# Kernel optimization log

Measured on AMD Instinct MI355X. Metric: run time of the kernel, lower is better.

The kernel has to match this reference:

```python
import jax, jax.numpy as jnp
import numpy as np

DIM = 4096
NH = 32       # query heads
NKV = 8       # kv heads
HD = DIM // NH  # 128
B = 1
S = 2048
ROPE_BASE = 10000.0


def rope_tables(seq_len, head_dim, base=ROPE_BASE):
    inv_freq = 1.0 / base ** (jnp.arange(0, head_dim, 2, dtype=jnp.float32) / head_dim)
    t = jnp.arange(seq_len, dtype=jnp.float32)
    freqs = jnp.einsum('i,j->ij', t, inv_freq)          # [S, HD/2]
    emb = jnp.concatenate([freqs, freqs], axis=-1)      # [S, HD]
    return jnp.cos(emb), jnp.sin(emb)


def apply_rope(x, cos, sin):
    # x: [B, H, S, HD]; matches torch apply_rotary_emb (chunk halves)
    x1, x2 = jnp.split(x, 2, axis=-1)
    d = x1.shape[-1]
    c = cos[None, None, :, :d]
    s = sin[None, None, :, :d]
    return jnp.concatenate([x1 * c - x2 * s, x2 * c + x1 * s], axis=-1)


def setup_inputs() -> dict:
    key = jax.random.key(0)
    k0, k1, k2, k3, k4 = jax.random.split(key, 5)
    sc = 0.02  # typical init scale for stable softmax
    return {
        'x': jax.random.normal(k0, (B, S, DIM), jnp.float32),
        'wq': jax.random.normal(k1, (DIM, NH * HD), jnp.float32) * sc,
        'wk': jax.random.normal(k2, (DIM, NKV * HD), jnp.float32) * sc,
        'wv': jax.random.normal(k3, (DIM, NKV * HD), jnp.float32) * sc,
        'wo': jax.random.normal(k4, (NH * HD, DIM), jnp.float32) * sc,
        'mask': jnp.ones((1,), jnp.bool_),  # presence triggers is_causal=True in torch SDPA path
    }


def reference(x, wq, wk, wv, wo, mask):
    Bsz, Sl, _ = x.shape
    n_rep = NH // NKV
    q = (x @ wq).reshape(Bsz, Sl, NH, HD).transpose(0, 2, 1, 3)    # [B,NH,S,HD]
    k = (x @ wk).reshape(Bsz, Sl, NKV, HD).transpose(0, 2, 1, 3)   # [B,NKV,S,HD]
    v = (x @ wv).reshape(Bsz, Sl, NKV, HD).transpose(0, 2, 1, 3)
    cos, sin = rope_tables(Sl, HD)
    q = apply_rope(q, cos, sin)
    k = apply_rope(k, cos, sin)
    # GQA without repeat_interleave: group query heads per kv head
    qg = q.reshape(Bsz, NKV, n_rep, Sl, HD)
    scale = HD ** -0.5
    scores = jnp.einsum('bgrqd,bgkd->bgrqk', qg, k) * scale        # [B,NKV,n_rep,S,S]
    causal = jnp.tril(jnp.ones((Sl, Sl), dtype=bool))
    scores = jnp.where(causal[None, None, None], scores, jnp.finfo(scores.dtype).min)
    attn = jax.nn.softmax(scores, axis=-1)
    out = jnp.einsum('bgrqk,bgkd->bgrqd', attn, v)                 # [B,NKV,n_rep,S,HD]
    out = out.reshape(Bsz, NH, Sl, HD).transpose(0, 2, 1, 3).reshape(Bsz, Sl, NH * HD)
    return out @ wo
```

## Files before the change

### kernel.cpp

```cpp
#include <hip/hip_runtime.h>
#include <hip/hip_bf16.h>
#include <cstdint>
#include <cmath>

#define DIM 4096
#define NH 32
#define NKV 8
#define HD 128
#define S_LEN 2048
#define KVD (NKV * HD)
#define QS 6144
#define SCALE 0.08838834764831845f

typedef __attribute__((ext_vector_type(4))) float f32x4;
typedef __attribute__((ext_vector_type(8))) short short8;

__device__ __forceinline__ short f2bf(float f) {
  union { float f; uint32_t u; } v; v.f = f;
  uint32_t u = v.u;
  u += 0x7fffu + ((u >> 16) & 1u);
  return (short)(u >> 16);
}
__device__ __forceinline__ float bf2f(short b) {
  union { uint32_t u; float f; } v; v.u = ((uint32_t)(uint16_t)b) << 16;
  return v.f;
}

__device__ __forceinline__ void async16(const void* g, void* l) {
  __builtin_amdgcn_global_load_lds(
      (__attribute__((address_space(1))) void*)(g),
      (__attribute__((address_space(3))) void*)(l), 16, 0, 0);
}


__global__ void rope_tables_k(float* __restrict__ ct, float* __restrict__ st) {
  const int i = blockIdx.x * blockDim.x + threadIdx.x;
  if (i >= S_LEN * 64) return;
  const int s = i >> 6, d = i & 63;
  const float inv = powf(10000.0f, -(float)(2 * d) / 128.0f);
  const float fr = (float)s * inv;
  ct[i] = cosf(fr);
  st[i] = sinf(fr);
}

__global__ void cast_f32_bf16_k(const float* __restrict__ in, short* __restrict__ out, int n4) {
  const int i = blockIdx.x * blockDim.x + threadIdx.x;
  if (i >= n4) return;
  const float4 v = ((const float4*)in)[i];
  short4 o;
  o.x = f2bf(v.x); o.y = f2bf(v.y); o.z = f2bf(v.z); o.w = f2bf(v.w);
  ((short4*)out)[i] = o;
}

__global__ __launch_bounds__(256) void prep_w_k(
    const float* __restrict__ wq, const float* __restrict__ wk,
    const float* __restrict__ wv, const float* __restrict__ wo,
    short* __restrict__ wqkvT, short* __restrict__ woT) {
  __shared__ float tile[64][65];
  int b = blockIdx.x;
  const float* src; short* dst; int N, bx, by;
  if (b < 4096)      { src = wq; dst = wqkvT;                        N = 4096; bx = b & 63; by = b >> 6; }
  else if (b < 5120) { b -= 4096; src = wk; dst = wqkvT + (size_t)4096 * DIM; N = 1024; bx = b & 15; by = b >> 4; }
  else if (b < 6144) { b -= 5120; src = wv; dst = wqkvT + (size_t)5120 * DIM; N = 1024; bx = b & 15; by = b >> 4; }
  else               { b -= 6144; src = wo; dst = woT;               N = 4096; bx = b & 63; by = b >> 6; }
  const int r0 = by * 64, c0 = bx * 64;
  const int t = threadIdx.x;
  const int lr = t >> 4, lc = (t & 15) * 4;
#pragma unroll
  for (int j = 0; j < 4; ++j) {
    const float4 v = *(const float4*)(src + (size_t)(r0 + lr + j * 16) * N + c0 + lc);
    tile[lr + j * 16][lc + 0] = v.x;
    tile[lr + j * 16][lc + 1] = v.y;
    tile[lr + j * 16][lc + 2] = v.z;
    tile[lr + j * 16][lc + 3] = v.w;
  }
  __syncthreads();
  const int orr = (t & 7) * 8;
  const int oc0 = t >> 3;
#pragma unroll
  for (int j = 0; j < 2; ++j) {
    const int oc = oc0 + j * 32;
    short8 o;
#pragma unroll
    for (int k = 0; k < 8; ++k) o[k] = f2bf(tile[orr + k][oc]);
    *(short8*)(dst + (size_t)(c0 + oc) * DIM + r0 + orr) = o;
  }
}

__global__ void transpose_bf16_k(const short* __restrict__ in, short* __restrict__ out,
                                 int R, int C, int ldi) {
  __shared__ short tile[32][33];
  const int tx = threadIdx.x, ty = threadIdx.y;
  const int c0 = blockIdx.x * 32, r0 = blockIdx.y * 32;
#pragma unroll
  for (int j = 0; j < 4; ++j)
    tile[ty + j * 8][tx] = in[(size_t)(r0 + ty + j * 8) * ldi + c0 + tx];
  __syncthreads();
#pragma unroll
  for (int j = 0; j < 4; ++j)
    out[(size_t)(c0 + ty + j * 8) * R + r0 + tx] = tile[tx][ty + j * 8];
}

__global__ void rope_apply_k(short* __restrict__ xq, int ld, const float* __restrict__ ct,
                             const float* __restrict__ st, int nheads) {
  const int i = blockIdx.x * blockDim.x + threadIdx.x;
  const int total = S_LEN * nheads * 64;
  if (i >= total) return;
  const int d = i & 63;
  const int t = i >> 6;
  const int hh = t % nheads;
  const int s = t / nheads;
  short* p = xq + (size_t)s * ld + hh * HD + d;
  const float x1 = bf2f(p[0]);
  const float x2 = bf2f(p[64]);
  const float c = ct[(s << 6) + d];
  const float sn = st[(s << 6) + d];
  p[0]  = f2bf(x1 * c - x2 * sn);
  p[64] = f2bf(x2 * c + x1 * sn);
}

#define SYNC2(VM, LG)                                            \
  asm volatile("s_waitcnt vmcnt(" #VM ")" ::: "memory");         \
  __builtin_amdgcn_s_barrier();                                  \
  asm volatile("s_waitcnt lgkmcnt(" #LG ")" ::: "memory");       \
  __builtin_amdgcn_sched_barrier(0);                             \
  __builtin_amdgcn_s_setprio(1)

#define PH_END()                                                 \
  __builtin_amdgcn_s_setprio(0);                                 \
  __builtin_amdgcn_sched_barrier(0);                             \
  __builtin_amdgcn_s_barrier()


__global__ __launch_bounds__(512, 2) void gemm192_k(
    const short* __restrict__ A, const short* __restrict__ BT,
    short* __restrict__ C, int M, int N, int K) {
  __shared__ __attribute__((aligned(16))) short ldsA[2][256 * 64];
  __shared__ __attribute__((aligned(16))) short ldsB[2][192 * 64];
  const int tid = threadIdx.x;
  const int l = tid & 63, w = tid >> 6;
  const int wrM = w >> 1, wcN = w & 1;
  const int lrow = l & 15, lg = l >> 4;
  const int cofs[2] = {(lg ^ (lrow & 7)) << 3, ((4 + lg) ^ (lrow & 7)) << 3};
  (void)M;

  int bid = blockIdx.x;
  const int cpx = gridDim.x >> 3;
  bid = (bid & 7) * cpx + (bid >> 3);
  const int ntn = N / 192;
  const int m0 = (bid / ntn) << 8;
  const int n0 = (bid % ntn) * 192;

  auto stageA = [&](int tau) {
    const int k0 = tau << 6;
    short* ad = &ldsA[tau & 1][0];
#pragma unroll
    for (int it = 0; it < 4; ++it) {
      const int e = it * 512 + tid;
      const int row = e >> 3;
      const int js = (e & 7) ^ (row & 7);
      async16(A + (size_t)(m0 + row) * K + k0 + js * 8, ad + e * 8);
    }
  };
  auto stageB = [&](int tau) {
    const int k0 = tau << 6;
    short* bd = &ldsB[tau & 1][0];
#pragma unroll
    for (int it = 0; it < 3; ++it) {
      const int e = it * 512 + tid;
      const int row = e >> 3;
      const int js = (e & 7) ^ (row & 7);
      async16(BT + (size_t)(n0 + row) * K + k0 + js * 8, bd + e * 8);
    }
  };
  auto rdA = [&](short8 (&dst)[4][2], int b) {
    const short* p = &ldsA[b][0];
#pragma unroll
    for (int mi = 0; mi < 4; ++mi) {
      const int row = wrM * 64 + mi * 16 + lrow;
#pragma unroll
      for (int kk = 0; kk < 2; ++kk)
        dst[mi][kk] = *(const short8*)(p + row * 64 + cofs[kk]);
    }
  };
  auto rdB3 = [&](short8 (&dst)[3][2], int b, int h) {
    const short* p = &ldsB[b][0];
#pragma unroll
    for (int ni = 0; ni < 3; ++ni) {
      const int row = wcN * 96 + h * 48 + ni * 16 + lrow;
#pragma unroll
      for (int kk = 0; kk < 2; ++kk)
        dst[ni][kk] = *(const short8*)(p + row * 64 + cofs[kk]);
    }
  };

  f32x4 acc[4][6] = {};
  auto half24 = [&](short8 (&Af)[4][2], int h, short8 (&Bf)[3][2]) {
#pragma unroll
    for (int kk = 0; kk < 2; ++kk)
#pragma unroll
      for (int mi = 0; mi < 4; ++mi)
#pragma unroll
        for (int ni = 0; ni < 3; ++ni)
          acc[mi][h * 3 + ni] = __builtin_amdgcn_mfma_f32_16x16x32_bf16(
              Af[mi][kk], Bf[ni][kk], acc[mi][h * 3 + ni], 0, 0, 0);
  };

  short8 Aa[4][2], Ab[4][2], BF[3][2], BS[3][2];

  stageA(0); stageB(0); stageA(1); stageB(1);
  asm volatile("s_waitcnt vmcnt(7)" ::: "memory");
  __builtin_amdgcn_s_barrier();
  rdA(Aa, 0); rdB3(BF, 0, 0);

  const int KT = K >> 6;
  for (int u = 0; u < (KT - 2) / 2; ++u) {
    const int e = 2 * u;
    rdB3(BS, 0, 1);
    SYNC2(7, 6);  stageA(e + 2); half24(Aa, 0, BF); PH_END();
    SYNC2(4, 0);  stageB(e + 2); rdA(Ab, 1); rdB3(BF, 1, 0);
                  half24(Aa, 1, BS); PH_END();
    rdB3(BS, 1, 1);
    SYNC2(7, 6);  stageA(e + 3); half24(Ab, 0, BF); PH_END();
    SYNC2(4, 0);  stageB(e + 3); rdA(Aa, 0); rdB3(BF, 0, 0);
                  half24(Ab, 1, BS); PH_END();
  }
  rdB3(BS, 0, 1);
  SYNC2(7, 6);  half24(Aa, 0, BF); PH_END();
  SYNC2(0, 0);  rdA(Ab, 1); rdB3(BF, 1, 0);
                half24(Aa, 1, BS); PH_END();
  rdB3(BS, 1, 1);
  SYNC2(0, 6);  half24(Ab, 0, BF); PH_END();
  SYNC2(0, 0);  half24(Ab, 1, BS); PH_END();

  const int orow0 = m0 + wrM * 64 + lg * 4;
  const int ocol0 = n0 + wcN * 96 + lrow;
#pragma unroll
  for (int mi = 0; mi < 4; ++mi)
#pragma unroll
    for (int n = 0; n < 6; ++n)
#pragma unroll
      for (int r = 0; r < 4; ++r)
        C[(size_t)(orow0 + mi * 16 + r) * N + (ocol0 + n * 16)] = f2bf(acc[mi][n][r]);
}


__global__ __launch_bounds__(512, 2) void gemm_wo2_k(
    const short* __restrict__ A, const short* __restrict__ BT,
    float* __restrict__ C, int M, int N, int K) {
  __shared__ __attribute__((aligned(16))) short ldsA[2][128 * 64];
  __shared__ __attribute__((aligned(16))) short ldsB[2][256 * 64];
  const int tid = threadIdx.x;
  const int l = tid & 63, w = tid >> 6;
  const int wrM = w >> 2, wcN = w & 3;
  const int lrow = l & 15, lg = l >> 4;
  const int cofs[2] = {(lg ^ (lrow & 7)) << 3, ((4 + lg) ^ (lrow & 7)) << 3};
  (void)M;

  int bid = blockIdx.x;
  const int cpx = gridDim.x >> 3;
  bid = (bid & 7) * cpx + (bid >> 3);
  const int ntn = N >> 8;
  const int m0 = (bid / ntn) << 7;
  const int n0 = (bid % ntn) << 8;

  auto stageA2 = [&](int tau) {
    const int k0 = tau << 6;
    short* ad = &ldsA[tau & 1][0];
#pragma unroll
    for (int it = 0; it < 2; ++it) {
      const int e = it * 512 + tid;
      const int row = e >> 3;
      const int js = (e & 7) ^ (row & 7);
      async16(A + (size_t)(m0 + row) * K + k0 + js * 8, ad + e * 8);
    }
  };
  auto stageB2 = [&](int tau) {
    const int k0 = tau << 6;
    short* bd = &ldsB[tau & 1][0];
#pragma unroll
    for (int it = 0; it < 4; ++it) {
      const int e = it * 512 + tid;
      const int row = e >> 3;
      const int js = (e & 7) ^ (row & 7);
      async16(BT + (size_t)(n0 + row) * K + k0 + js * 8, bd + e * 8);
    }
  };
  auto rdA = [&](short8 (&dst)[4][2], int b) {
    const short* p = &ldsA[b][0];
#pragma unroll
    for (int mi = 0; mi < 4; ++mi) {
      const int row = wrM * 64 + mi * 16 + lrow;
#pragma unroll
      for (int kk = 0; kk < 2; ++kk)
        dst[mi][kk] = *(const short8*)(p + row * 64 + cofs[kk]);
    }
  };
  auto rdB = [&](short8 (&dst)[2][2], int b, int h) {
    const short* p = &ldsB[b][0];
#pragma unroll
    for (int ni = 0; ni < 2; ++ni) {
      const int row = wcN * 64 + h * 32 + ni * 16 + lrow;
#pragma unroll
      for (int kk = 0; kk < 2; ++kk)
        dst[ni][kk] = *(const short8*)(p + row * 64 + cofs[kk]);
    }
  };

  f32x4 acc[4][4] = {};
  auto half = [&](short8 (&Af)[4][2], int h, short8 (&Bf)[2][2]) {
#pragma unroll
    for (int kk = 0; kk < 2; ++kk)
#pragma unroll
      for (int mi = 0; mi < 4; ++mi)
#pragma unroll
        for (int ni = 0; ni < 2; ++ni)
          acc[mi][h * 2 + ni] = __builtin_amdgcn_mfma_f32_16x16x32_bf16(
              Af[mi][kk], Bf[ni][kk], acc[mi][h * 2 + ni], 0, 0, 0);
  };

  short8 Aa[4][2], Ab[4][2], H0[2][2], H1[2][2];

  stageA2(0); stageB2(0); stageA2(1); stageB2(1);
  asm volatile("s_waitcnt vmcnt(6)" ::: "memory");
  __builtin_amdgcn_s_barrier();
  rdA(Aa, 0); rdB(H0, 0, 0);

  const int KT = K >> 6;
  for (int u = 0; u < (KT - 2) / 2; ++u) {
    const int e = 2 * u;
    rdB(H1, 0, 1);
    SYNC2(6, 4);  stageA2(e + 2); half(Aa, 0, H0); PH_END();
    SYNC2(2, 0);  stageB2(e + 2); rdA(Ab, 1); rdB(H0, 1, 0);
                  half(Aa, 1, H1); PH_END();
    rdB(H1, 1, 1);
    SYNC2(6, 4);  stageA2(e + 3); half(Ab, 0, H0); PH_END();
    SYNC2(2, 0);  stageB2(e + 3); rdA(Aa, 0); rdB(H0, 0, 0);
                  half(Ab, 1, H1); PH_END();
  }
  rdB(H1, 0, 1);
  SYNC2(6, 4);  half(Aa, 0, H0); PH_END();
  SYNC2(0, 0);  rdA(Ab, 1); rdB(H0, 1, 0);
                half(Aa, 1, H1); PH_END();
  rdB(H1, 1, 1);
  SYNC2(0, 4);  half(Ab, 0, H0); PH_END();
  SYNC2(0, 0);  half(Ab, 1, H1); PH_END();

  const int orow0 = m0 + wrM * 64 + lg * 4;
  const int ocol0 = n0 + wcN * 64 + lrow;
#pragma unroll
  for (int mi = 0; mi < 4; ++mi)
#pragma unroll
    for (int n = 0; n < 4; ++n)
#pragma unroll
      for (int r = 0; r < 4; ++r)
        C[(size_t)(orow0 + mi * 16 + r) * N + (ocol0 + n * 16)] = acc[mi][n][r];
}


__global__ __launch_bounds__(256, 3) void attn_k(
    const short* __restrict__ Q, const short* __restrict__ Kc,
    const short* __restrict__ VTg, short* __restrict__ O) {
  __shared__ __attribute__((aligned(16))) short Ks[2][64 * 128];
  __shared__ __attribute__((aligned(16))) short Vt[2][128 * 64];
  __shared__ __attribute__((aligned(16))) short Ps[4][32 * 64];

  const int tid = threadIdx.x;
  const int w = tid >> 6, l = tid & 63;
  const int lrow = l & 15, lg = l >> 4;

  int b = blockIdx.x, h, qt;
  if (b < 256) { h = b >> 3; qt = 15 - (b & 7); }
  else { b -= 256; h = b >> 3; qt = b & 7; }
  const int kvh = h >> 2;
  const int qb0 = qt * 128;
  const int qrow0 = qb0 + w * 32;
  const int nkt = 2 * qt + 2;

  short8 qf[2][4];
#pragma unroll
  for (int nq = 0; nq < 2; ++nq) {
    const short* qp = Q + (size_t)(qrow0 + nq * 16 + lrow) * QS + h * HD;
#pragma unroll
    for (int c = 0; c < 4; ++c) qf[nq][c] = *(const short8*)(qp + c * 32 + lg * 8);
  }

  f32x4 o_acc[2][8] = {};
  float m[2] = {-INFINITY, -INFINITY};
  float lsum[2] = {0.f, 0.f};

  auto stage = [&](int kb, int buf) {
    short* kd = Ks[buf];
    short* vd = Vt[buf];
#pragma unroll
    for (int it = 0; it < 4; ++it) {
      const int e = it * 256 + tid;
      const int row = e >> 4, j = e & 15;
      const int jsrc = (j & 8) | ((j ^ row) & 7);
      async16(Kc + (size_t)(kb + row) * QS + kvh * HD + jsrc * 8, kd + e * 8);
    }
#pragma unroll
    for (int it = 0; it < 4; ++it) {
      const int e = it * 256 + tid;
      const int d = e >> 3, j = e & 7;
      const int jsrc = (j ^ d) & 7;
      async16(VTg + (size_t)(kvh * HD + d) * S_LEN + kb + jsrc * 8, vd + e * 8);
    }
  };

  stage(0, 0);
  int cur = 0;

  for (int kt = 0; kt < nkt; ++kt) {
    __syncthreads();
    if (kt + 1 < nkt) stage((kt + 1) * 64, cur ^ 1);
    const int kb = kt * 64;

    if (kb <= qrow0 + 31) {
      const char* ks = (const char*)Ks[cur];
      const char* vt = (const char*)Vt[cur];
      char* psb = (char*)Ps[w];

      f32x4 stq[4][2] = {};
#pragma unroll
      for (int c = 0; c < 4; ++c) {
#pragma unroll
        for (int mk = 0; mk < 4; ++mk) {
          const short8 kf = *(const short8*)(
              ks + (mk * 16 + lrow) * 256 + (((c * 4 + lg) ^ (lrow & 7)) << 4));
          stq[mk][0] = __builtin_amdgcn_mfma_f32_16x16x32_bf16(kf, qf[0][c], stq[mk][0], 0, 0, 0);
          stq[mk][1] = __builtin_amdgcn_mfma_f32_16x16x32_bf16(kf, qf[1][c], stq[mk][1], 0, 0, 0);
        }
      }

      const bool needmask = (kb + 63 > qrow0);
#pragma unroll
      for (int mk = 0; mk < 4; ++mk)
#pragma unroll
        for (int nq = 0; nq < 2; ++nq)
#pragma unroll
          for (int r = 0; r < 4; ++r) {
            float v = stq[mk][nq][r] * SCALE;
            if (needmask && (kb + mk * 16 + lg * 4 + r > qrow0 + nq * 16 + lrow))
              v = -INFINITY;
            stq[mk][nq][r] = v;
          }

      float vmax[2];
#pragma unroll
      for (int nq = 0; nq < 2; ++nq) {
        float v = stq[0][nq][0];
#pragma unroll
        for (int mk = 0; mk < 4; ++mk)
#pragma unroll
          for (int r = 0; r < 4; ++r) v = fmaxf(v, stq[mk][nq][r]);
        v = fmaxf(v, __shfl_xor(v, 16));
        v = fmaxf(v, __shfl_xor(v, 32));
        vmax[nq] = v;
      }

      const int small = (vmax[0] <= m[0] + 8.0f) && (vmax[1] <= m[1] + 8.0f);
      if (!__all(small)) {
        float al[2];
#pragma unroll
        for (int nq = 0; nq < 2; ++nq) {
          const float mn = fmaxf(m[nq], vmax[nq]);
          al[nq] = __expf(m[nq] - mn);
          m[nq] = mn;
          lsum[nq] *= al[nq];
        }
#pragma unroll
        for (int mmq = 0; mmq < 2; ++mmq)
#pragma unroll
          for (int r = 0; r < 4; ++r) {
            const float a = __shfl(al[mmq], lg * 4 + r);
#pragma unroll
            for (int d = 0; d < 8; ++d) o_acc[mmq][d][r] *= a;
          }
      }

      float rs[2] = {0.f, 0.f};
#pragma unroll
      for (int nq = 0; nq < 2; ++nq) {
#pragma unroll
        for (int mk = 0; mk < 4; ++mk) {
          const float p0 = __expf(stq[mk][nq][0] - m[nq]);
          const float p1 = __expf(stq[mk][nq][1] - m[nq]);
          const float p2 = __expf(stq[mk][nq][2] - m[nq]);
          const float p3 = __expf(stq[mk][nq][3] - m[nq]);
          rs[nq] += (p0 + p1) + (p2 + p3);
          __hip_bfloat16 b0 = __float2bfloat16(p0), b1 = __float2bfloat16(p1);
          __hip_bfloat16 b2 = __float2bfloat16(p2), b3 = __float2bfloat16(p3);
          short4 pk;
          pk.x = *(short*)&b0; pk.y = *(short*)&b1; pk.z = *(short*)&b2; pk.w = *(short*)&b3;
          const int q = nq * 16 + lrow;
          *(short4*)(psb + q * 128 + ((mk * 32 + lg * 8) ^ ((q & 7) << 4))) = pk;
        }
        float r2 = rs[nq];
        r2 += __shfl_xor(r2, 16);
        r2 += __shfl_xor(r2, 32);
        lsum[nq] += r2;
      }

#pragma unroll
      for (int cc = 0; cc < 2; ++cc) {
        const int chunk = ((cc * 4 + lg) ^ (lrow & 7)) << 4;
        const short8 pa0 = *(const short8*)(psb + lrow * 128 + chunk);
        const short8 pa1 = *(const short8*)(psb + (16 + lrow) * 128 + chunk);
#pragma unroll
        for (int d = 0; d < 8; ++d) {
          const short8 vf = *(const short8*)(vt + (d * 16 + lrow) * 128 + chunk);
          o_acc[0][d] = __builtin_amdgcn_mfma_f32_16x16x32_bf16(pa0, vf, o_acc[0][d], 0, 0, 0);
          o_acc[1][d] = __builtin_amdgcn_mfma_f32_16x16x32_bf16(pa1, vf, o_acc[1][d], 0, 0, 0);
        }
      }
    }
    cur ^= 1;
  }

  float linv[2] = {1.0f / lsum[0], 1.0f / lsum[1]};
#pragma unroll
  for (int mmq = 0; mmq < 2; ++mmq)
#pragma unroll
    for (int r = 0; r < 4; ++r) {
      const float li = __shfl(linv[mmq], lg * 4 + r);
      short* op = O + (size_t)(qrow0 + mmq * 16 + lg * 4 + r) * DIM + h * HD;
#pragma unroll
      for (int d = 0; d < 8; ++d)
        op[d * 16 + lrow] = f2bf(o_acc[mmq][d][r] * li);
    }
}


extern "C" void kernel_launch(void* const* d_in, const int* in_sizes, int n_in,
                              void* d_out, int out_size, void* d_ws, size_t ws_size,
                              hipStream_t stream) {
  const float* x  = (const float*)d_in[0];
  const float* wq = (const float*)d_in[1];
  const float* wk = (const float*)d_in[2];
  const float* wv = (const float*)d_in[3];
  const float* wo = (const float*)d_in[4];
  float* out = (float*)d_out;
  (void)in_sizes; (void)n_in; (void)out_size; (void)ws_size;

  char* ws = (char*)d_ws;
  size_t off = 0;
  auto alloc = [&](size_t bytes) -> void* {
    void* p = ws + off;
    off += (bytes + 255) & ~(size_t)255;
    return p;
  };
  short* xb     = (short*)alloc((size_t)S_LEN * DIM * 2);
  short* wqkvT  = (short*)alloc((size_t)QS * DIM * 2);
  short* woT    = (short*)alloc((size_t)DIM * DIM * 2);
  short* qkv    = (short*)alloc((size_t)S_LEN * QS * 2);
  short* vtg    = (short*)alloc((size_t)KVD * S_LEN * 2);
  short* ao     = (short*)alloc((size_t)S_LEN * DIM * 2);
  float* ct     = (float*)alloc((size_t)S_LEN * 64 * 4);
  float* st     = (float*)alloc((size_t)S_LEN * 64 * 4);

  rope_tables_k<<<(S_LEN * 64) / 256, 256, 0, stream>>>(ct, st);
  cast_f32_bf16_k<<<(S_LEN * DIM / 4) / 256, 256, 0, stream>>>(x, xb, S_LEN * DIM / 4);
  prep_w_k<<<dim3(10240), dim3(256), 0, stream>>>(wq, wk, wv, wo, wqkvT, woT);

  gemm192_k<<<dim3((S_LEN / 256) * (QS / 192)), 512, 0, stream>>>(
      xb, wqkvT, qkv, S_LEN, QS, DIM);

  rope_apply_k<<<(S_LEN * 40 * 64) / 256, 256, 0, stream>>>(qkv, QS, ct, st, 40);

  transpose_bf16_k<<<dim3(KVD / 32, S_LEN / 32), dim3(32, 8), 0, stream>>>(
      qkv + 5120, vtg, S_LEN, KVD, QS);

  attn_k<<<dim3(512), 256, 0, stream>>>(qkv, qkv + 4096, vtg, ao);

  gemm_wo2_k<<<dim3((S_LEN / 128) * (DIM / 256)), 512, 0, stream>>>(
      ao, woT, out, S_LEN, DIM, DIM);
}
```

Before: 318.6 us.

## Restructure GEMM main loops to batch global staging and double-buffer B fragments

Reworks the software pipeline in the QKV and output-projection GEMM kernels. Global-to-LDS staging for A and B is now issued together in one phase. The second-half B fragments get their own double-buffered register sets, so all LDS reads for the next half are issued a full phase early. The wait counts in the barrier macros change to match. This aims to hide LDS read latency and cut the number of distinct wait points, at the cost of more registers, which could hurt occupancy.

```diff
diff --git a/kernel.cpp b/kernel.cpp
--- a/kernel.cpp
+++ b/kernel.cpp
@@ -206,32 +206,30 @@
               Af[mi][kk], Bf[ni][kk], acc[mi][h * 3 + ni], 0, 0, 0);
   };
 
-  short8 Aa[4][2], Ab[4][2], BF[3][2], BS[3][2];
+  short8 Aa[4][2], Ab[4][2], BF[3][2], BSa[3][2], BSb[3][2];
 
   stageA(0); stageB(0); stageA(1); stageB(1);
   asm volatile("s_waitcnt vmcnt(7)" ::: "memory");
   __builtin_amdgcn_s_barrier();
-  rdA(Aa, 0); rdB3(BF, 0, 0);
+  rdA(Aa, 0); rdB3(BF, 0, 0); rdB3(BSa, 0, 1);
 
   const int KT = K >> 6;
   for (int u = 0; u < (KT - 2) / 2; ++u) {
     const int e = 2 * u;
-    rdB3(BS, 0, 1);
-    SYNC2(7, 6);  stageA(e + 2); half24(Aa, 0, BF); PH_END();
-    SYNC2(4, 0);  stageB(e + 2); rdA(Ab, 1); rdB3(BF, 1, 0);
-                  half24(Aa, 1, BS); PH_END();
-    rdB3(BS, 1, 1);
-    SYNC2(7, 6);  stageA(e + 3); half24(Ab, 0, BF); PH_END();
-    SYNC2(4, 0);  stageB(e + 3); rdA(Aa, 0); rdB3(BF, 0, 0);
-                  half24(Ab, 1, BS); PH_END();
+    SYNC2(7, 0);  stageA(e + 2); stageB(e + 2);
+                  half24(Aa, 0, BF); PH_END();
+    SYNC2(7, 0);  rdA(Ab, 1); rdB3(BF, 1, 0); rdB3(BSb, 1, 1);
+                  half24(Aa, 1, BSa); PH_END();
+    SYNC2(7, 0);  stageA(e + 3); stageB(e + 3);
+                  half24(Ab, 0, BF); PH_END();
+    SYNC2(7, 0);  rdA(Aa, 0); rdB3(BF, 0, 0); rdB3(BSa, 0, 1);
+                  half24(Ab, 1, BSb); PH_END();
   }
-  rdB3(BS, 0, 1);
-  SYNC2(7, 6);  half24(Aa, 0, BF); PH_END();
-  SYNC2(0, 0);  rdA(Ab, 1); rdB3(BF, 1, 0);
-                half24(Aa, 1, BS); PH_END();
-  rdB3(BS, 1, 1);
-  SYNC2(0, 6);  half24(Ab, 0, BF); PH_END();
-  SYNC2(0, 0);  half24(Ab, 1, BS); PH_END();
+  SYNC2(7, 0);  half24(Aa, 0, BF); PH_END();
+  SYNC2(0, 0);  rdA(Ab, 1); rdB3(BF, 1, 0); rdB3(BSb, 1, 1);
+                half24(Aa, 1, BSa); PH_END();
+  SYNC2(0, 0);  half24(Ab, 0, BF); PH_END();
+  SYNC2(0, 0);  half24(Ab, 1, BSb); PH_END();
 
   const int orow0 = m0 + wrM * 64 + lg * 4;
   const int ocol0 = n0 + wcN * 96 + lrow;
@@ -319,32 +317,30 @@
               Af[mi][kk], Bf[ni][kk], acc[mi][h * 2 + ni], 0, 0, 0);
   };
 
-  short8 Aa[4][2], Ab[4][2], H0[2][2], H1[2][2];
+  short8 Aa[4][2], Ab[4][2], H0[2][2], H1a[2][2], H1b[2][2];
 
   stageA2(0); stageB2(0); stageA2(1); stageB2(1);
   asm volatile("s_waitcnt vmcnt(6)" ::: "memory");
   __builtin_amdgcn_s_barrier();
-  rdA(Aa, 0); rdB(H0, 0, 0);
+  rdA(Aa, 0); rdB(H0, 0, 0); rdB(H1a, 0, 1);
 
   const int KT = K >> 6;
   for (int u = 0; u < (KT - 2) / 2; ++u) {
     const int e = 2 * u;
-    rdB(H1, 0, 1);
-    SYNC2(6, 4);  stageA2(e + 2); half(Aa, 0, H0); PH_END();
-    SYNC2(2, 0);  stageB2(e + 2); rdA(Ab, 1); rdB(H0, 1, 0);
-                  half(Aa, 1, H1); PH_END();
-    rdB(H1, 1, 1);
-    SYNC2(6, 4);  stageA2(e + 3); half(Ab, 0, H0); PH_END();
-    SYNC2(2, 0);  stageB2(e + 3); rdA(Aa, 0); rdB(H0, 0, 0);
-                  half(Ab, 1, H1); PH_END();
+    SYNC2(6, 0);  stageA2(e + 2); stageB2(e + 2);
+                  half(Aa, 0, H0); PH_END();
+    SYNC2(6, 0);  rdA(Ab, 1); rdB(H0, 1, 0); rdB(H1b, 1, 1);
+                  half(Aa, 1, H1a); PH_END();
+    SYNC2(6, 0);  stageA2(e + 3); stageB2(e + 3);
+                  half(Ab, 0, H0); PH_END();
+    SYNC2(6, 0);  rdA(Aa, 0); rdB(H0, 0, 0); rdB(H1a, 0, 1);
+                  half(Ab, 1, H1b); PH_END();
   }
-  rdB(H1, 0, 1);
-  SYNC2(6, 4);  half(Aa, 0, H0); PH_END();
-  SYNC2(0, 0);  rdA(Ab, 1); rdB(H0, 1, 0);
-                half(Aa, 1, H1); PH_END();
-  rdB(H1, 1, 1);
-  SYNC2(0, 4);  half(Ab, 0, H0); PH_END();
-  SYNC2(0, 0);  half(Ab, 1, H1); PH_END();
+  SYNC2(6, 0);  half(Aa, 0, H0); PH_END();
+  SYNC2(0, 0);  rdA(Ab, 1); rdB(H0, 1, 0); rdB(H1b, 1, 1);
+                half(Aa, 1, H1a); PH_END();
+  SYNC2(0, 0);  half(Ab, 0, H0); PH_END();
+  SYNC2(0, 0);  half(Ab, 1, H1b); PH_END();
 
   const int orow0 = m0 + wrM * 64 + lg * 4;
   const int ocol0 = n0 + wcN * 64 + lrow;
```

Result: no change. 312.9 us (-1.8%).
